# Kernel tuning notes

Hardware: AMD Instinct MI355X
Metric: run time of the kernel (lower is better)

The kernel has to match this reference:

```python
import jax, jax.numpy as jnp
import numpy as np

N_TOKENS = 32768
DIM = 2048
N_EXPERTS = 256
N_GROUPS = 8
N_LIMITED_GROUPS = 4
TOP_K = 8
ROUTE_SCALE = 2.5


def setup_inputs() -> dict:
    key = jax.random.key(0)
    k1, k2, k3, k4 = jax.random.split(key, 4)
    x = jax.random.normal(k1, (N_TOKENS, DIM), dtype=jnp.float32)
    w1 = jax.random.normal(k2, (N_EXPERTS, DIM), dtype=jnp.float32) * (DIM ** -0.5)
    b_lin = jax.random.normal(k3, (N_EXPERTS,), dtype=jnp.float32) * 0.02
    bias = jax.random.normal(k4, (N_EXPERTS,), dtype=jnp.float32) * 0.02
    return {"x": x, "w1": w1, "b_lin": b_lin, "bias": bias}


def reference(x, w1, b_lin, bias):
    n = x.shape[0]
    # gate GEMM: [N, dim] x [dim, E] -> [N, E]
    logits = jnp.einsum("nd,ed->ne", x, w1) + b_lin
    # sigmoid scoring with L1 normalization
    s = jax.nn.sigmoid(logits)
    s = s / jnp.sum(s, axis=-1, keepdims=True)
    # routing-correction bias (torch code adds it in place, so it is also in the
    # gathered values via the original_scores alias)
    s = s + bias
    original_scores = s
    # group-limited masking: keep only top n_limited_groups groups (amax score,
    # since use_bias=True)
    g = s.reshape(n, N_GROUPS, N_EXPERTS // N_GROUPS)
    group_scores = jnp.max(g, axis=-1)                      # [N, G]
    _, gidx = jax.lax.top_k(group_scores, N_LIMITED_GROUPS)  # [N, Glim]
    keep = jnp.zeros((n, N_GROUPS), dtype=bool).at[
        jnp.arange(n)[:, None], gidx].set(True)
    masked = jnp.where(keep[:, :, None], g, -jnp.inf).reshape(n, N_EXPERTS)
    # final top-k over masked scores, gather from (bias-added) original scores
    _, indices = jax.lax.top_k(masked, TOP_K)               # [N, k]
    values = jnp.take_along_axis(original_scores, indices, axis=1) * ROUTE_SCALE
    return values.astype(x.dtype), indices
```

## Files before the change

kernel.cpp:

```cpp
#include <hip/hip_runtime.h>
#include <math.h>

#define NTOK   32768
#define DIM    2048
#define NE     256
#define NG     8
#define GSZ    32
#define NLIM   4
#define TOPK   8
#define RSCALE 2.5f
#define TAU    4e-7f

#define BT      64
#define THREADS 256
#define KT      16
#define NKT     (DIM / KT)
#define WOFF    262144
#define TILE_B  16384

typedef __bf16 bf16x8 __attribute__((ext_vector_type(8)));
typedef float  f32x16 __attribute__((ext_vector_type(16)));

typedef const __attribute__((address_space(1))) void GASV;
typedef __attribute__((address_space(3))) void LASV;

__device__ __forceinline__ void gload16(const void* g, void* l) {
    __builtin_amdgcn_global_load_lds((GASV*)g, (LASV*)l, 16, 0, 0);
}

__global__ __launch_bounds__(256) void wsplit_kernel(
    const float* __restrict__ w1, unsigned int* __restrict__ wt)
{
    const int g  = blockIdx.x * 256 + threadIdx.x;
    const int e  = g & 255;
    const int hi = (g >> 8) & 1;
    const int p  = (g >> 9) & 1;
    const int kt = g >> 10;
    const float* src = w1 + (size_t)e * DIM + kt * 16 + hi * 8;

    uint4 o;
    unsigned int w[4];
#pragma unroll
    for (int q = 0; q < 4; ++q) {
        const float v0 = src[2 * q], v1 = src[2 * q + 1];
        const unsigned int u0 = __float_as_uint(v0);
        const unsigned int u1 = __float_as_uint(v1);
        if (p == 0) {
            w[q] = (u0 >> 16) | (u1 & 0xFFFF0000u);
        } else {
            const float r0 = v0 - __uint_as_float(u0 & 0xFFFF0000u);
            const float r1 = v1 - __uint_as_float(u1 & 0xFFFF0000u);
            w[q] = (__float_as_uint(r0) >> 16) |
                   (__float_as_uint(r1) & 0xFFFF0000u);
        }
    }
    o.x = w[0]; o.y = w[1]; o.z = w[2]; o.w = w[3];
    *(uint4*)(wt + (size_t)g * 4) = o;
}

__global__ __launch_bounds__(THREADS, 2) void router_pass1(
    const float* __restrict__ x, const unsigned int* __restrict__ wt,
    const float* __restrict__ b_lin, const float* __restrict__ bias,
    float* __restrict__ out_vals, float* __restrict__ out_idx,
    int* __restrict__ wsI)
{
    __shared__ union {
        struct {
            alignas(16) char B[3 * TILE_B];
            float xs[2][16][72];
        } t;
        float sc[32 * 260];
    } sm;

    const int tid  = threadIdx.x;
    const int lane = tid & 63;
    const int wave = tid >> 6;
    const int l31  = lane & 31;
    const int hi   = lane >> 5;
    const int wm   = wave >> 1;
    const int wn   = wave & 1;
    const int t0   = blockIdx.x * BT;

    const int xtr = tid >> 2, xkq = tid & 3;
    const float* xgp = x + (size_t)(t0 + xtr) * DIM + xkq * 4;
    const int acol = wm * 32 + l31;

    const char* wsrc = (const char*)wt;
    char* bc = sm.t.B;
    char* bn = sm.t.B + TILE_B;
    char* bs = sm.t.B + 2 * TILE_B;

    auto STAGE = [&](char* ldsbase, int kt) {
#pragma unroll
        for (int q = 0; q < 4; ++q) {
            const int chunk = wave * 4 + q;
            gload16(wsrc + (size_t)kt * TILE_B + chunk * 1024 + lane * 16,
                    ldsbase + chunk * 1024);
        }
    };
    auto XWRITE = [&](int b, float4 v) {
        sm.t.xs[b][xkq * 4 + 0][xtr] = v.x;
        sm.t.xs[b][xkq * 4 + 1][xtr] = v.y;
        sm.t.xs[b][xkq * 4 + 2][xtr] = v.z;
        sm.t.xs[b][xkq * 4 + 3][xtr] = v.w;
    };
    auto AFRAG = [&](int b, bf16x8& ah, bf16x8& ar) {
        union { unsigned int u[4]; bf16x8 v; } H, R;
#pragma unroll
        for (int q = 0; q < 4; ++q) {
            const float f0 = sm.t.xs[b][hi * 8 + 2 * q][acol];
            const float f1 = sm.t.xs[b][hi * 8 + 2 * q + 1][acol];
            const unsigned int u0 = __float_as_uint(f0);
            const unsigned int u1 = __float_as_uint(f1);
            H.u[q] = (u0 >> 16) | (u1 & 0xFFFF0000u);
            const float r0 = f0 - __uint_as_float(u0 & 0xFFFF0000u);
            const float r1 = f1 - __uint_as_float(u1 & 0xFFFF0000u);
            R.u[q] = (__float_as_uint(r0) >> 16) |
                     (__float_as_uint(r1) & 0xFFFF0000u);
        }
        ah = H.v; ar = R.v;
    };

    f32x16 acc[4] = {};
    const int e_base = (wn * 128 + l31) * 16;
    const int hi4k   = hi * 4096;

    float4 rA, rB;

    rA = *(const float4*)xgp;
    __builtin_amdgcn_sched_barrier(0);
    STAGE(bc, 0);
    __builtin_amdgcn_sched_barrier(0);
    rB = *(const float4*)(xgp + KT);
    __builtin_amdgcn_sched_barrier(0);
    STAGE(bn, 1);
    __builtin_amdgcn_sched_barrier(0);
    asm volatile("s_waitcnt vmcnt(9)");
    __builtin_amdgcn_sched_barrier(0);
    XWRITE(0, rA);

    auto ITER = [&](int kt, float4 wrv, float4& ldv, bool last) {
        if (!last) asm volatile("s_waitcnt vmcnt(4)");
        else       asm volatile("s_waitcnt vmcnt(0)");
        __builtin_amdgcn_sched_barrier(0);
        asm volatile("s_waitcnt lgkmcnt(0)");
        __builtin_amdgcn_sched_barrier(0);
        __builtin_amdgcn_s_barrier();
        __builtin_amdgcn_sched_barrier(0);
        if (kt + 1 < NKT) XWRITE((kt + 1) & 1, wrv);
        if (kt + 2 < NKT) ldv = *(const float4*)(xgp + (kt + 2) * KT);
        __builtin_amdgcn_sched_barrier(0);
        if (kt + 2 < NKT) STAGE(bs, kt + 2);
        __builtin_amdgcn_sched_barrier(0);

        bf16x8 ah, ar;
        AFRAG(kt & 1, ah, ar);
        __builtin_amdgcn_s_setprio(1);
#pragma unroll
        for (int j = 0; j < 4; ++j) {
            const int eo = e_base + j * 512;
            bf16x8 bh = *(const bf16x8*)(bc + hi4k + eo);
            bf16x8 br = *(const bf16x8*)(bc + 8192 + hi4k + eo);
            acc[j] = __builtin_amdgcn_mfma_f32_32x32x16_bf16(ah, bh, acc[j], 0, 0, 0);
            acc[j] = __builtin_amdgcn_mfma_f32_32x32x16_bf16(ah, br, acc[j], 0, 0, 0);
            acc[j] = __builtin_amdgcn_mfma_f32_32x32x16_bf16(ar, bh, acc[j], 0, 0, 0);
        }
        __builtin_amdgcn_s_setprio(0);
        char* t = bc; bc = bn; bn = bs; bs = t;
    };

    for (int kt2 = 0; kt2 < NKT - 4; kt2 += 2) {
        ITER(kt2,     rB, rA, false);
        ITER(kt2 + 1, rA, rB, false);
    }
    ITER(NKT - 4, rB, rA, false);
    ITER(NKT - 3, rA, rB, false);
    ITER(NKT - 2, rB, rA, false);
    ITER(NKT - 1, rA, rB, true);

    __syncthreads();

    const int tx = tid & 31;
    const int ty = tid >> 5;
    float blv[8], bsv[8];
#pragma unroll
    for (int j = 0; j < 8; ++j) {
        blv[j] = b_lin[tx + 32 * j];
        bsv[j] = bias[tx + 32 * j];
    }

    for (int h = 0; h < 2; ++h) {
        if (h) __syncthreads();
        if (wm == h) {
#pragma unroll
            for (int j = 0; j < 4; ++j) {
#pragma unroll
                for (int r = 0; r < 16; ++r) {
                    const int row = (r & 3) + 8 * (r >> 2) + 4 * hi;
                    const int e   = wn * 128 + j * 32 + l31;
                    sm.sc[row * 260 + e] = acc[j][r];
                }
            }
        }
        __syncthreads();

#pragma unroll
        for (int i = 0; i < 4; ++i) {
            const int row = ty * 4 + i;
            float s8[8];
            float psum = 0.0f;
#pragma unroll
            for (int j = 0; j < 8; ++j) {
                const float lg = sm.sc[row * 260 + tx + 32 * j] + blv[j];
                const float s = 1.0f / (1.0f + expf(-lg));
                s8[j] = s;
                psum += s;
            }
#pragma unroll
            for (int m = 1; m <= 16; m <<= 1) psum += __shfl_xor(psum, m);
#pragma unroll
            for (int j = 0; j < 8; ++j) s8[j] = s8[j] / psum + bsv[j];

            float gm[8];
#pragma unroll
            for (int j = 0; j < 8; ++j) gm[j] = s8[j];
#pragma unroll
            for (int m = 1; m <= 16; m <<= 1)
#pragma unroll
                for (int j = 0; j < 8; ++j)
                    gm[j] = fmaxf(gm[j], __shfl_xor(gm[j], m));

            unsigned keep = 0u;
            float g4v = 0.0f, g5v = 0.0f;
#pragma unroll
            for (int r = 0; r < 5; ++r) {
                float bv = -1e30f; int bg = 0;
#pragma unroll
                for (int g = 0; g < 8; ++g)
                    if (!((keep >> g) & 1) && gm[g] > bv) { bv = gm[g]; bg = g; }
                if (r < 4) { keep |= 1u << bg; g4v = bv; }
                else g5v = bv;
            }
            float margin = g4v - g5v;

#pragma unroll
            for (int j = 0; j < 8; ++j)
                if (!((keep >> j) & 1)) s8[j] = -1e30f;

            float tv[9]; int te[9];
#pragma unroll
            for (int r = 0; r < 9; ++r) {
                float bv = -1e30f; int bj = 8;
#pragma unroll
                for (int j = 0; j < 8; ++j)
                    if (s8[j] > bv) { bv = s8[j]; bj = j; }
                int be = (bj < 8) ? (tx + 32 * bj) : 9999;
#pragma unroll
                for (int m = 1; m <= 16; m <<= 1) {
                    const float ov = __shfl_xor(bv, m);
                    const int   oe = __shfl_xor(be, m);
                    if (ov > bv || (ov == bv && oe < be)) { bv = ov; be = oe; }
                }
                tv[r] = bv; te[r] = be;
                if (r < 8 && (be & 31) == tx) s8[be >> 5] = -1e30f;
            }
#pragma unroll
            for (int r = 0; r < 8; ++r) margin = fminf(margin, tv[r] - tv[r + 1]);

            if (tx == 0) {
                const int t = t0 + h * 32 + row;
                const int base = t * TOPK;
#pragma unroll
                for (int r = 0; r < 8; ++r) {
                    out_vals[base + r] = tv[r] * RSCALE;
                    out_idx[base + r]  = (float)te[r];
                }
                if (margin < TAU) {
                    const int slot = atomicAdd(&wsI[0], 1);
                    if (slot < 60000) wsI[4 + slot] = t;
                }
            }
        }
    }
}

__global__ __launch_bounds__(THREADS, 1) void router_pass2(
    const float* __restrict__ x, const float* __restrict__ w1,
    const float* __restrict__ b_lin, const float* __restrict__ bias,
    float* __restrict__ out_vals, float* __restrict__ out_idx,
    const int* __restrict__ wsI)
{
    __shared__ double xrow[DIM];
    __shared__ double red[256];
    __shared__ double sc[NE];

    const int tid = threadIdx.x;
    const int count = min(wsI[0], 60000);
    const int* list = wsI + 4;
    const float4* x4 = (const float4*)x;
    const float4* w4 = (const float4*)w1;

    for (int li = blockIdx.x; li < count; li += gridDim.x) {
        const int t = list[li];
        __syncthreads();
#pragma unroll
        for (int q = 0; q < 2; ++q) {
            const int id = tid + 256 * q;
            const float4 v = x4[t * 512 + id];
            xrow[id * 4 + 0] = (double)v.x;
            xrow[id * 4 + 1] = (double)v.y;
            xrow[id * 4 + 2] = (double)v.z;
            xrow[id * 4 + 3] = (double)v.w;
        }
        __syncthreads();

        const int e = tid;
        double a0 = 0.0, a1 = 0.0, a2 = 0.0, a3 = 0.0;
#pragma unroll 2
        for (int k4 = 0; k4 < 512; k4 += 4) {
#pragma unroll
            for (int z = 0; z < 4; ++z) {
                const float4 wv = w4[e * 512 + k4 + z];
                double* ac = (z == 0) ? &a0 : (z == 1) ? &a1 : (z == 2) ? &a2 : &a3;
                *ac = fma(xrow[(k4 + z) * 4 + 0], (double)wv.x, *ac);
                *ac = fma(xrow[(k4 + z) * 4 + 1], (double)wv.y, *ac);
                *ac = fma(xrow[(k4 + z) * 4 + 2], (double)wv.z, *ac);
                *ac = fma(xrow[(k4 + z) * 4 + 3], (double)wv.w, *ac);
            }
        }
        const double lg = ((a0 + a1) + (a2 + a3)) + (double)b_lin[e];
        const double s = 1.0 / (1.0 + exp(-lg));
        red[tid] = s;
        __syncthreads();
        for (int off = 128; off > 0; off >>= 1) {
            if (tid < off) red[tid] += red[tid + off];
            __syncthreads();
        }
        sc[e] = s / red[0] + (double)bias[e];
        __syncthreads();

        if (tid == 0) {
            double gmax[NG];
            for (int g = 0; g < NG; ++g) {
                double mx = -INFINITY;
                for (int q = 0; q < GSZ; ++q) {
                    const double v = sc[g * GSZ + q];
                    mx = (v > mx) ? v : mx;
                }
                gmax[g] = mx;
            }
            unsigned keep = 0u;
            for (int r = 0; r < NLIM; ++r) {
                int best = 0; double bv = -INFINITY;
                for (int g = 0; g < NG; ++g) {
                    if (keep & (1u << g)) continue;
                    if (gmax[g] > bv) { bv = gmax[g]; best = g; }
                }
                keep |= 1u << best;
            }
            double tv[TOPK]; int ti[TOPK];
            for (int r = 0; r < TOPK; ++r) { tv[r] = -INFINITY; ti[r] = NE; }
            for (int g = 0; g < NG; ++g) {
                if (!(keep & (1u << g))) continue;
                for (int q = 0; q < GSZ; ++q) {
                    const int ee = g * GSZ + q;
                    const double v = sc[ee];
                    if (v > tv[TOPK - 1]) {
                        int p = TOPK - 1;
                        while (p > 0 && v > tv[p - 1]) {
                            tv[p] = tv[p - 1]; ti[p] = ti[p - 1]; --p;
                        }
                        tv[p] = v; ti[p] = ee;
                    }
                }
            }
            const int base = t * TOPK;
            for (int r = 0; r < TOPK; ++r) {
                out_vals[base + r] = (float)(tv[r] * (double)RSCALE);
                out_idx[base + r]  = (float)ti[r];
            }
        }
    }
}

extern "C" void kernel_launch(void* const* d_in, const int* in_sizes, int n_in,
                              void* d_out, int out_size, void* d_ws, size_t ws_size,
                              hipStream_t stream) {
    const float* x     = (const float*)d_in[0];
    const float* w1    = (const float*)d_in[1];
    const float* b_lin = (const float*)d_in[2];
    const float* bias  = (const float*)d_in[3];
    float* out_vals = (float*)d_out;
    float* out_idx  = (float*)d_out + (size_t)NTOK * TOPK;

    int* wsI = (int*)d_ws;
    unsigned int* wt = (unsigned int*)((char*)d_ws + WOFF);

    hipMemsetAsync(d_ws, 0, 16, stream);
    wsplit_kernel<<<dim3(512), 256, 0, stream>>>(w1, wt);
    router_pass1<<<dim3(NTOK / BT), THREADS, 0, stream>>>(
        x, wt, b_lin, bias, out_vals, out_idx, wsI);
    router_pass2<<<dim3(256), THREADS, 0, stream>>>(
        x, w1, b_lin, bias, out_vals, out_idx, (const int*)d_ws);
}
```

Baseline: 261.2 us.

## Enlarge router GEMM tile to 128 tokens with 512 threads and K=32 steps

Grows the block tile from 64 to 128 tokens and the block from 256 to 512 threads (8 waves as 2x4). Each wave now computes a 64x64 sub-tile with a 2x2 MFMA register block, so every B fragment loaded from LDS serves two A fragments. K per pipeline step doubles to 32, which halves the number of barriers and staging rounds, and x is stored as float2 pairs. The cost is more LDS per block (about 96KB of B buffers), probably lower occupancy, and a post-GEMM epilogue that now needs four serialized shared-memory rounds.

```diff
diff --git a/kernel.cpp b/kernel.cpp
--- a/kernel.cpp
+++ b/kernel.cpp
@@ -11,12 +11,11 @@
 #define RSCALE 2.5f
 #define TAU    4e-7f
 
-#define BT      64
-#define THREADS 256
-#define KT      16
-#define NKT     (DIM / KT)
+#define BT      128
+#define THREADS 512
+#define NIT     (DIM / 32)
 #define WOFF    262144
-#define TILE_B  16384
+#define TILE_B  32768
 
 typedef __bf16 bf16x8 __attribute__((ext_vector_type(8)));
 typedef float  f32x16 __attribute__((ext_vector_type(16)));
@@ -67,7 +66,7 @@
     __shared__ union {
         struct {
             alignas(16) char B[3 * TILE_B];
-            float xs[2][16][72];
+            float2 xs[2][16][128];
         } t;
         float sc[32 * 260];
     } sm;
@@ -77,13 +76,12 @@
     const int wave = tid >> 6;
     const int l31  = lane & 31;
     const int hi   = lane >> 5;
-    const int wm   = wave >> 1;
-    const int wn   = wave & 1;
+    const int wm   = wave >> 2;
+    const int wn   = wave & 3;
     const int t0   = blockIdx.x * BT;
 
     const int xtr = tid >> 2, xkq = tid & 3;
-    const float* xgp = x + (size_t)(t0 + xtr) * DIM + xkq * 4;
-    const int acol = wm * 32 + l31;
+    const float4* xg4 = (const float4*)(x + (size_t)(t0 + xtr) * DIM) + xkq * 2;
 
     const char* wsrc = (const char*)wt;
     char* bc = sm.t.B;
@@ -98,85 +96,90 @@
                     ldsbase + chunk * 1024);
         }
     };
-    auto XWRITE = [&](int b, float4 v) {
-        sm.t.xs[b][xkq * 4 + 0][xtr] = v.x;
-        sm.t.xs[b][xkq * 4 + 1][xtr] = v.y;
-        sm.t.xs[b][xkq * 4 + 2][xtr] = v.z;
-        sm.t.xs[b][xkq * 4 + 3][xtr] = v.w;
+    auto XWRITE = [&](int b, float4 v0, float4 v1) {
+        const int kp0 = xkq * 4;
+        sm.t.xs[b][kp0 + 0][xtr] = make_float2(v0.x, v0.y);
+        sm.t.xs[b][kp0 + 1][xtr] = make_float2(v0.z, v0.w);
+        sm.t.xs[b][kp0 + 2][xtr] = make_float2(v1.x, v1.y);
+        sm.t.xs[b][kp0 + 3][xtr] = make_float2(v1.z, v1.w);
     };
-    auto AFRAG = [&](int b, bf16x8& ah, bf16x8& ar) {
+    auto AFRAG = [&](int b, int s16, int mi, bf16x8& ah, bf16x8& ar) {
+        const int tok = wm * 64 + mi * 32 + l31;
         union { unsigned int u[4]; bf16x8 v; } H, R;
 #pragma unroll
         for (int q = 0; q < 4; ++q) {
-            const float f0 = sm.t.xs[b][hi * 8 + 2 * q][acol];
-            const float f1 = sm.t.xs[b][hi * 8 + 2 * q + 1][acol];
-            const unsigned int u0 = __float_as_uint(f0);
-            const unsigned int u1 = __float_as_uint(f1);
+            const float2 f = sm.t.xs[b][s16 * 8 + hi * 4 + q][tok];
+            const unsigned int u0 = __float_as_uint(f.x);
+            const unsigned int u1 = __float_as_uint(f.y);
             H.u[q] = (u0 >> 16) | (u1 & 0xFFFF0000u);
-            const float r0 = f0 - __uint_as_float(u0 & 0xFFFF0000u);
-            const float r1 = f1 - __uint_as_float(u1 & 0xFFFF0000u);
+            const float r0 = f.x - __uint_as_float(u0 & 0xFFFF0000u);
+            const float r1 = f.y - __uint_as_float(u1 & 0xFFFF0000u);
             R.u[q] = (__float_as_uint(r0) >> 16) |
                      (__float_as_uint(r1) & 0xFFFF0000u);
         }
         ah = H.v; ar = R.v;
     };
 
-    f32x16 acc[4] = {};
-    const int e_base = (wn * 128 + l31) * 16;
-    const int hi4k   = hi * 4096;
-
-    float4 rA, rB;
-
-    rA = *(const float4*)xgp;
+    f32x16 acc[2][2] = {};
+    const int beo = hi * 4096 + (wn * 64 + l31) * 16;
+
+    float4 rA0, rA1, rB0, rB1;
+
+    rA0 = xg4[0]; rA1 = xg4[1];
     __builtin_amdgcn_sched_barrier(0);
     STAGE(bc, 0);
     __builtin_amdgcn_sched_barrier(0);
-    rB = *(const float4*)(xgp + KT);
+    rB0 = xg4[8]; rB1 = xg4[9];
     __builtin_amdgcn_sched_barrier(0);
     STAGE(bn, 1);
     __builtin_amdgcn_sched_barrier(0);
-    asm volatile("s_waitcnt vmcnt(9)");
+    asm volatile("s_waitcnt vmcnt(10)");
     __builtin_amdgcn_sched_barrier(0);
-    XWRITE(0, rA);
-
-    auto ITER = [&](int kt, float4 wrv, float4& ldv, bool last) {
-        if (!last) asm volatile("s_waitcnt vmcnt(4)");
-        else       asm volatile("s_waitcnt vmcnt(0)");
+    XWRITE(0, rA0, rA1);
+
+    auto ITER = [&](int kt, float4 w0, float4 w1, float4& l0, float4& l1) {
+        if (kt < NIT - 1) asm volatile("s_waitcnt vmcnt(4)");
+        else              asm volatile("s_waitcnt vmcnt(0)");
         __builtin_amdgcn_sched_barrier(0);
         asm volatile("s_waitcnt lgkmcnt(0)");
         __builtin_amdgcn_sched_barrier(0);
         __builtin_amdgcn_s_barrier();
         __builtin_amdgcn_sched_barrier(0);
-        if (kt + 1 < NKT) XWRITE((kt + 1) & 1, wrv);
-        if (kt + 2 < NKT) ldv = *(const float4*)(xgp + (kt + 2) * KT);
-        __builtin_amdgcn_sched_barrier(0);
-        if (kt + 2 < NKT) STAGE(bs, kt + 2);
-        __builtin_amdgcn_sched_barrier(0);
-
-        bf16x8 ah, ar;
-        AFRAG(kt & 1, ah, ar);
-        __builtin_amdgcn_s_setprio(1);
-#pragma unroll
-        for (int j = 0; j < 4; ++j) {
-            const int eo = e_base + j * 512;
-            bf16x8 bh = *(const bf16x8*)(bc + hi4k + eo);
-            bf16x8 br = *(const bf16x8*)(bc + 8192 + hi4k + eo);
-            acc[j] = __builtin_amdgcn_mfma_f32_32x32x16_bf16(ah, bh, acc[j], 0, 0, 0);
-            acc[j] = __builtin_amdgcn_mfma_f32_32x32x16_bf16(ah, br, acc[j], 0, 0, 0);
-            acc[j] = __builtin_amdgcn_mfma_f32_32x32x16_bf16(ar, bh, acc[j], 0, 0, 0);
-        }
-        __builtin_amdgcn_s_setprio(0);
+        if (kt + 1 < NIT) XWRITE((kt + 1) & 1, w0, w1);
+        __builtin_amdgcn_sched_barrier(0);
+        if (kt + 2 < NIT) { l0 = xg4[(kt + 2) * 8]; l1 = xg4[(kt + 2) * 8 + 1]; }
+        __builtin_amdgcn_sched_barrier(0);
+        if (kt + 2 < NIT) STAGE(bs, kt + 2);
+        __builtin_amdgcn_sched_barrier(0);
+
+        const int b = kt & 1;
+#pragma unroll
+        for (int s16 = 0; s16 < 2; ++s16) {
+            bf16x8 ah0, ar0, ah1, ar1;
+            AFRAG(b, s16, 0, ah0, ar0);
+            AFRAG(b, s16, 1, ah1, ar1);
+            __builtin_amdgcn_s_setprio(1);
+#pragma unroll
+            for (int ni = 0; ni < 2; ++ni) {
+                const char* pb = bc + s16 * 16384 + ni * 512 + beo;
+                bf16x8 bh = *(const bf16x8*)(pb);
+                bf16x8 br = *(const bf16x8*)(pb + 8192);
+                acc[0][ni] = __builtin_amdgcn_mfma_f32_32x32x16_bf16(ah0, bh, acc[0][ni], 0, 0, 0);
+                acc[0][ni] = __builtin_amdgcn_mfma_f32_32x32x16_bf16(ah0, br, acc[0][ni], 0, 0, 0);
+                acc[0][ni] = __builtin_amdgcn_mfma_f32_32x32x16_bf16(ar0, bh, acc[0][ni], 0, 0, 0);
+                acc[1][ni] = __builtin_amdgcn_mfma_f32_32x32x16_bf16(ah1, bh, acc[1][ni], 0, 0, 0);
+                acc[1][ni] = __builtin_amdgcn_mfma_f32_32x32x16_bf16(ah1, br, acc[1][ni], 0, 0, 0);
+                acc[1][ni] = __builtin_amdgcn_mfma_f32_32x32x16_bf16(ar1, bh, acc[1][ni], 0, 0, 0);
+            }
+            __builtin_amdgcn_s_setprio(0);
+        }
         char* t = bc; bc = bn; bn = bs; bs = t;
     };
 
-    for (int kt2 = 0; kt2 < NKT - 4; kt2 += 2) {
-        ITER(kt2,     rB, rA, false);
-        ITER(kt2 + 1, rA, rB, false);
+    for (int kt = 0; kt < NIT; kt += 2) {
+        ITER(kt,     rB0, rB1, rA0, rA1);
+        ITER(kt + 1, rA0, rA1, rB0, rB1);
     }
-    ITER(NKT - 4, rB, rA, false);
-    ITER(NKT - 3, rA, rB, false);
-    ITER(NKT - 2, rB, rA, false);
-    ITER(NKT - 1, rA, rB, true);
 
     __syncthreads();
 
@@ -189,24 +192,25 @@
         bsv[j] = bias[tx + 32 * j];
     }
 
-    for (int h = 0; h < 2; ++h) {
-        if (h) __syncthreads();
-        if (wm == h) {
-#pragma unroll
-            for (int j = 0; j < 4; ++j) {
+    for (int qq = 0; qq < 4; ++qq) {
+        if (qq) __syncthreads();
+        if (wm == (qq >> 1)) {
+            const int mi = qq & 1;
+#pragma unroll
+            for (int ni = 0; ni < 2; ++ni) {
 #pragma unroll
                 for (int r = 0; r < 16; ++r) {
                     const int row = (r & 3) + 8 * (r >> 2) + 4 * hi;
-                    const int e   = wn * 128 + j * 32 + l31;
-                    sm.sc[row * 260 + e] = acc[j][r];
+                    const int e   = wn * 64 + ni * 32 + l31;
+                    sm.sc[row * 260 + e] = acc[mi][ni][r];
                 }
             }
         }
         __syncthreads();
 
 #pragma unroll
-        for (int i = 0; i < 4; ++i) {
-            const int row = ty * 4 + i;
+        for (int i = 0; i < 2; ++i) {
+            const int row = ty * 2 + i;
             float s8[8];
             float psum = 0.0f;
 #pragma unroll
@@ -268,7 +272,7 @@
             for (int r = 0; r < 8; ++r) margin = fminf(margin, tv[r] - tv[r + 1]);
 
             if (tx == 0) {
-                const int t = t0 + h * 32 + row;
+                const int t = t0 + qq * 32 + row;
                 const int base = t * TOPK;
 #pragma unroll
                 for (int r = 0; r < 8; ++r) {
@@ -284,7 +288,7 @@
     }
 }
 
-__global__ __launch_bounds__(THREADS, 1) void router_pass2(
+__global__ __launch_bounds__(256, 1) void router_pass2(
     const float* __restrict__ x, const float* __restrict__ w1,
     const float* __restrict__ b_lin, const float* __restrict__ bias,
     float* __restrict__ out_vals, float* __restrict__ out_idx,
@@ -400,6 +404,6 @@
     wsplit_kernel<<<dim3(512), 256, 0, stream>>>(w1, wt);
     router_pass1<<<dim3(NTOK / BT), THREADS, 0, stream>>>(
         x, wt, b_lin, bias, out_vals, out_idx, wsI);
-    router_pass2<<<dim3(256), THREADS, 0, stream>>>(
+    router_pass2<<<dim3(256), 256, 0, stream>>>(
         x, w1, b_lin, bias, out_vals, out_idx, (const int*)d_ws);
 }
```

After: 314.8 us. 20.5% more time.
